# Kernel tuning notes

Measured on AMD Instinct MI355X. Metric: run time of the kernel, lower is better.

Reference implementation:

```python
import jax, jax.numpy as jnp
import numpy as np

EPS = 1e-10
FAR_DELTA = 1e10  # delta appended for the last sample, as in the torch code


def setup_inputs() -> dict:
    key = jax.random.key(0)
    k1, k2, k3 = jax.random.split(key, 3)
    N, P, C = 131072, 128, 3
    density = jax.random.normal(k1, (N, P), dtype=jnp.float32)  # raw density (relu'd inside)
    feature = jax.random.uniform(k2, (N, P, C), dtype=jnp.float32)
    # depth values must be increasing along the sample dim (they come from a ray sampler);
    # build them as a cumulative sum of positive steps in roughly [0, 6].
    steps = jax.random.uniform(k3, (N, P), dtype=jnp.float32) * 0.05
    depth_values = jnp.cumsum(steps, axis=-1) + 1.0
    return {"density": density, "feature": feature, "depth_values": depth_values}


def reference(density, feature, depth_values):
    # deltas: consecutive depth differences, huge delta for the final sample  [N, P]
    deltas = jnp.concatenate(
        [depth_values[:, 1:] - depth_values[:, :-1],
         jnp.full_like(depth_values[:, :1], FAR_DELTA)], axis=-1)
    # alpha = 1 - exp(-relu(density) * delta)   [N, P]
    alpha = 1.0 - jnp.exp(-jax.nn.relu(density) * deltas)
    # transmittance: exclusive cumprod of (1 - alpha + eps)   [N, P]
    trans = jnp.cumprod(
        jnp.concatenate([jnp.ones_like(alpha[:, :1]), 1.0 - alpha + EPS], axis=-1),
        axis=-1)[:, :-1]
    weights = alpha * trans  # [N, P]
    feat_out = jnp.sum(weights[..., None] * feature, axis=1)  # [N, C]
    depth_out = jnp.sum(weights * depth_values, axis=1)       # [N]
    return feat_out, depth_out
```

## Files before the change

kernel.cpp:

```cpp
#include <hip/hip_runtime.h>

#define EPS 1e-10f
#define FAR_DELTA 1e10f

template<int CTRL>
__device__ __forceinline__ float dpp_mov(float x, float old) {
    return __int_as_float(__builtin_amdgcn_update_dpp(
        __float_as_int(old), __float_as_int(x), CTRL, 0xF, 0xF, false));
}

__global__ __launch_bounds__(256) void volrend_kernel(
    const float* __restrict__ density,
    const float* __restrict__ feature,
    const float* __restrict__ depth,
    float* __restrict__ feat_out,
    float* __restrict__ depth_out,
    int N)
{
    const int tid  = threadIdx.x;
    const int lane = tid & 63;
    const int wv   = tid >> 6;
    const int j    = lane & 15;
    const int sub  = lane >> 4;
    const int ray  = blockIdx.x * 16 + wv * 4 + sub;
    if (ray >= N) return;

    const float4* d4 = (const float4*)(density + (size_t)ray * 128 + j * 8);
    const float4* z4 = (const float4*)(depth   + (size_t)ray * 128 + j * 8);
    const float4* f4 = (const float4*)(feature + (size_t)ray * 384 + j * 24);

    float4 dA = d4[0], dB = d4[1];
    float4 zA = z4[0], zB = z4[1];
    float4 F0 = f4[0], F1 = f4[1], F2 = f4[2], F3 = f4[3], F4 = f4[4], F5 = f4[5];

    float z[8]  = {zA.x, zA.y, zA.z, zA.w, zB.x, zB.y, zB.z, zB.w};
    float dn[8] = {dA.x, dA.y, dA.z, dA.w, dB.x, dB.y, dB.z, dB.w};

    float znext = dpp_mov<0x101>(z[0], 0.0f);

    float al[8], tt[8];
    #pragma unroll
    for (int k = 0; k < 8; ++k) {
        float delta = (k < 7) ? (z[k + 1] - z[k])
                              : ((j == 15) ? FAR_DELTA : (znext - z[7]));
        float ex = __expf(-fmaxf(dn[k], 0.0f) * delta);
        al[k] = 1.0f - ex;
        tt[k] = ex + EPS;
    }

    float loc = tt[0];
    #pragma unroll
    for (int k = 1; k < 8; ++k) loc *= tt[k];

    float s = loc;
    s *= dpp_mov<0x111>(s, 1.0f);
    s *= dpp_mov<0x112>(s, 1.0f);
    s *= dpp_mov<0x114>(s, 1.0f);
    s *= dpp_mov<0x118>(s, 1.0f);
    float excl = dpp_mov<0x111>(s, 1.0f);

    float f[24] = {F0.x, F0.y, F0.z, F0.w, F1.x, F1.y, F1.z, F1.w,
                   F2.x, F2.y, F2.z, F2.w, F3.x, F3.y, F3.z, F3.w,
                   F4.x, F4.y, F4.z, F4.w, F5.x, F5.y, F5.z, F5.w};

    float trans = excl;
    float a0 = 0.0f, a1 = 0.0f, a2 = 0.0f, ad = 0.0f;
    #pragma unroll
    for (int k = 0; k < 8; ++k) {
        float wk = al[k] * trans;
        trans *= tt[k];
        a0 += wk * f[3 * k + 0];
        a1 += wk * f[3 * k + 1];
        a2 += wk * f[3 * k + 2];
        ad += wk * z[k];
    }

    a0 += dpp_mov<0x128>(a0, 0.0f);
    a1 += dpp_mov<0x128>(a1, 0.0f);
    a2 += dpp_mov<0x128>(a2, 0.0f);
    ad += dpp_mov<0x128>(ad, 0.0f);
    a0 += dpp_mov<0x124>(a0, 0.0f);
    a1 += dpp_mov<0x124>(a1, 0.0f);
    a2 += dpp_mov<0x124>(a2, 0.0f);
    ad += dpp_mov<0x124>(ad, 0.0f);
    a0 += dpp_mov<0x122>(a0, 0.0f);
    a1 += dpp_mov<0x122>(a1, 0.0f);
    a2 += dpp_mov<0x122>(a2, 0.0f);
    ad += dpp_mov<0x122>(ad, 0.0f);
    a0 += dpp_mov<0x121>(a0, 0.0f);
    a1 += dpp_mov<0x121>(a1, 0.0f);
    a2 += dpp_mov<0x121>(a2, 0.0f);
    ad += dpp_mov<0x121>(ad, 0.0f);

    if (j == 0) {
        feat_out[(size_t)ray * 3 + 0] = a0;
        feat_out[(size_t)ray * 3 + 1] = a1;
        feat_out[(size_t)ray * 3 + 2] = a2;
        depth_out[ray] = ad;
    }
}

extern "C" void kernel_launch(void* const* d_in, const int* in_sizes, int n_in,
                              void* d_out, int out_size, void* d_ws, size_t ws_size,
                              hipStream_t stream) {
    const float* density = (const float*)d_in[0];
    const float* feature = (const float*)d_in[1];
    const float* depth   = (const float*)d_in[2];

    const int P = 128;
    const int N = in_sizes[0] / P;

    float* feat_out  = (float*)d_out;
    float* depth_out = (float*)d_out + (size_t)N * 3;

    dim3 grid((N + 15) / 16);
    dim3 block(256);
    volrend_kernel<<<grid, block, 0, stream>>>(density, feature, depth,
                                               feat_out, depth_out, N);
}
```

Baseline: 351.3 us.

## Coalesce global loads via split sample layout and LDS-staged feature tile

Each lane now owns samples j*4..j*4+3 and 64+j*4..64+j*4+3, so density and depth loads are contiguous across lanes. Features for the wave's four rays are loaded with a fully coalesced linear pattern, staged through LDS, and read back per lane. The transmittance scan is split into two 16-lane scans, and the upper half is stitched to the lower half's total with a shuffle. The aim is better memory coalescing for a bandwidth-bound kernel, at the cost of LDS traffic and extra scan and shuffle work. The LDS reads happen without an explicit barrier, which relies on all lanes of a wave executing in lockstep.

```diff
diff --git a/kernel.cpp b/kernel.cpp
--- a/kernel.cpp
+++ b/kernel.cpp
@@ -2,6 +2,8 @@
 
 #define EPS 1e-10f
 #define FAR_DELTA 1e10f
+
+typedef float f4v __attribute__((ext_vector_type(4)));
 
 template<int CTRL>
 __device__ __forceinline__ float dpp_mov(float x, float old) {
@@ -17,62 +19,118 @@
     float* __restrict__ depth_out,
     int N)
 {
+    __shared__ float lds[4 * 1536];
+
     const int tid  = threadIdx.x;
     const int lane = tid & 63;
     const int wv   = tid >> 6;
     const int j    = lane & 15;
     const int sub  = lane >> 4;
-    const int ray  = blockIdx.x * 16 + wv * 4 + sub;
+    const int ray0 = blockIdx.x * 16 + wv * 4;
+    const int ray  = ray0 + sub;
     if (ray >= N) return;
 
-    const float4* d4 = (const float4*)(density + (size_t)ray * 128 + j * 8);
-    const float4* z4 = (const float4*)(depth   + (size_t)ray * 128 + j * 8);
-    const float4* f4 = (const float4*)(feature + (size_t)ray * 384 + j * 24);
+    const float* dp = density + (size_t)ray * 128;
+    const float* zp = depth   + (size_t)ray * 128;
+    f4v dA = *(const f4v*)(dp + j * 4);
+    f4v dB = *(const f4v*)(dp + 64 + j * 4);
+    f4v zA = *(const f4v*)(zp + j * 4);
+    f4v zB = *(const f4v*)(zp + 64 + j * 4);
 
-    float4 dA = d4[0], dB = d4[1];
-    float4 zA = z4[0], zB = z4[1];
-    float4 F0 = f4[0], F1 = f4[1], F2 = f4[2], F3 = f4[3], F4 = f4[4], F5 = f4[5];
+    const float* fsrc = feature + (size_t)ray0 * 384;
+    float* flds = lds + wv * 1536;
+    f4v FR0 = *(const f4v*)(fsrc + 0 * 256 + lane * 4);
+    f4v FR1 = *(const f4v*)(fsrc + 1 * 256 + lane * 4);
+    f4v FR2 = *(const f4v*)(fsrc + 2 * 256 + lane * 4);
+    f4v FR3 = *(const f4v*)(fsrc + 3 * 256 + lane * 4);
+    f4v FR4 = *(const f4v*)(fsrc + 4 * 256 + lane * 4);
+    f4v FR5 = *(const f4v*)(fsrc + 5 * 256 + lane * 4);
+    *(f4v*)(flds + 0 * 256 + lane * 4) = FR0;
+    *(f4v*)(flds + 1 * 256 + lane * 4) = FR1;
+    *(f4v*)(flds + 2 * 256 + lane * 4) = FR2;
+    *(f4v*)(flds + 3 * 256 + lane * 4) = FR3;
+    *(f4v*)(flds + 4 * 256 + lane * 4) = FR4;
+    *(f4v*)(flds + 5 * 256 + lane * 4) = FR5;
 
-    float z[8]  = {zA.x, zA.y, zA.z, zA.w, zB.x, zB.y, zB.z, zB.w};
-    float dn[8] = {dA.x, dA.y, dA.z, dA.w, dB.x, dB.y, dB.z, dB.w};
+    float zlo[4] = {zA.x, zA.y, zA.z, zA.w};
+    float zhi[4] = {zB.x, zB.y, zB.z, zB.w};
+    float nlo[4] = {dA.x, dA.y, dA.z, dA.w};
+    float nhi[4] = {dB.x, dB.y, dB.z, dB.w};
 
-    float znext = dpp_mov<0x101>(z[0], 0.0f);
+    float znlo = dpp_mov<0x101>(zlo[0], 0.0f);
+    float znhi = dpp_mov<0x101>(zhi[0], 0.0f);
+    float z64  = __shfl(zhi[0], 0, 16);
 
-    float al[8], tt[8];
+    float allo[4], ttlo[4], alhi[4], tthi[4];
     #pragma unroll
-    for (int k = 0; k < 8; ++k) {
-        float delta = (k < 7) ? (z[k + 1] - z[k])
-                              : ((j == 15) ? FAR_DELTA : (znext - z[7]));
-        float ex = __expf(-fmaxf(dn[k], 0.0f) * delta);
-        al[k] = 1.0f - ex;
-        tt[k] = ex + EPS;
+    for (int k = 0; k < 4; ++k) {
+        float dz = (k < 3) ? (zlo[k + 1] - zlo[k])
+                           : (((j == 15) ? z64 : znlo) - zlo[3]);
+        float ex = __expf(-fmaxf(nlo[k], 0.0f) * dz);
+        allo[k] = 1.0f - ex;
+        ttlo[k] = ex + EPS;
+    }
+    #pragma unroll
+    for (int k = 0; k < 4; ++k) {
+        float dz = (k < 3) ? (zhi[k + 1] - zhi[k])
+                           : ((j == 15) ? FAR_DELTA : (znhi - zhi[3]));
+        float ex = __expf(-fmaxf(nhi[k], 0.0f) * dz);
+        alhi[k] = 1.0f - ex;
+        tthi[k] = ex + EPS;
     }
 
-    float loc = tt[0];
-    #pragma unroll
-    for (int k = 1; k < 8; ++k) loc *= tt[k];
+    float plo = ttlo[0] * ttlo[1] * ttlo[2] * ttlo[3];
+    float phi = tthi[0] * tthi[1] * tthi[2] * tthi[3];
 
-    float s = loc;
-    s *= dpp_mov<0x111>(s, 1.0f);
-    s *= dpp_mov<0x112>(s, 1.0f);
-    s *= dpp_mov<0x114>(s, 1.0f);
-    s *= dpp_mov<0x118>(s, 1.0f);
-    float excl = dpp_mov<0x111>(s, 1.0f);
+    float slo = plo;
+    slo *= dpp_mov<0x111>(slo, 1.0f);
+    slo *= dpp_mov<0x112>(slo, 1.0f);
+    slo *= dpp_mov<0x114>(slo, 1.0f);
+    slo *= dpp_mov<0x118>(slo, 1.0f);
+    float exlo = dpp_mov<0x111>(slo, 1.0f);
 
-    float f[24] = {F0.x, F0.y, F0.z, F0.w, F1.x, F1.y, F1.z, F1.w,
-                   F2.x, F2.y, F2.z, F2.w, F3.x, F3.y, F3.z, F3.w,
-                   F4.x, F4.y, F4.z, F4.w, F5.x, F5.y, F5.z, F5.w};
+    float shi = phi;
+    shi *= dpp_mov<0x111>(shi, 1.0f);
+    shi *= dpp_mov<0x112>(shi, 1.0f);
+    shi *= dpp_mov<0x114>(shi, 1.0f);
+    shi *= dpp_mov<0x118>(shi, 1.0f);
+    float exhi_l = dpp_mov<0x111>(shi, 1.0f);
 
-    float trans = excl;
+    float Tlo  = __shfl(slo, 15, 16);
+    float exhi = Tlo * exhi_l;
+
+    const float* fl = flds + sub * 384 + j * 12;
+    f4v g0 = *(const f4v*)(fl + 0);
+    f4v g1 = *(const f4v*)(fl + 4);
+    f4v g2 = *(const f4v*)(fl + 8);
+    f4v h0 = *(const f4v*)(fl + 192);
+    f4v h1 = *(const f4v*)(fl + 196);
+    f4v h2 = *(const f4v*)(fl + 200);
+
     float a0 = 0.0f, a1 = 0.0f, a2 = 0.0f, ad = 0.0f;
-    #pragma unroll
-    for (int k = 0; k < 8; ++k) {
-        float wk = al[k] * trans;
-        trans *= tt[k];
-        a0 += wk * f[3 * k + 0];
-        a1 += wk * f[3 * k + 1];
-        a2 += wk * f[3 * k + 2];
-        ad += wk * z[k];
+    {
+        float t = exlo;
+        float w0 = allo[0] * t; t *= ttlo[0];
+        float w1 = allo[1] * t; t *= ttlo[1];
+        float w2 = allo[2] * t; t *= ttlo[2];
+        float w3 = allo[3] * t;
+        a0 += w0 * g0.x; a1 += w0 * g0.y; a2 += w0 * g0.z;
+        a0 += w1 * g0.w; a1 += w1 * g1.x; a2 += w1 * g1.y;
+        a0 += w2 * g1.z; a1 += w2 * g1.w; a2 += w2 * g2.x;
+        a0 += w3 * g2.y; a1 += w3 * g2.z; a2 += w3 * g2.w;
+        ad += w0 * zlo[0] + w1 * zlo[1] + w2 * zlo[2] + w3 * zlo[3];
+    }
+    {
+        float t = exhi;
+        float w0 = alhi[0] * t; t *= tthi[0];
+        float w1 = alhi[1] * t; t *= tthi[1];
+        float w2 = alhi[2] * t; t *= tthi[2];
+        float w3 = alhi[3] * t;
+        a0 += w0 * h0.x; a1 += w0 * h0.y; a2 += w0 * h0.z;
+        a0 += w1 * h0.w; a1 += w1 * h1.x; a2 += w1 * h1.y;
+        a0 += w2 * h1.z; a1 += w2 * h1.w; a2 += w2 * h2.x;
+        a0 += w3 * h2.y; a1 += w3 * h2.z; a2 += w3 * h2.w;
+        ad += w0 * zhi[0] + w1 * zhi[1] + w2 * zhi[2] + w3 * zhi[3];
     }
 
     a0 += dpp_mov<0x128>(a0, 0.0f);
```

Measured after the change: 353.6 us. Within noise of the previous version (+0.7%).
